# Kernel optimization log

Hardware: AMD Instinct MI355X
Metric: run time of the kernel (lower is better)

Reference implementation:

```python
import jax, jax.numpy as jnp
import numpy as np

FP8_MAX = 448.0  # max representable magnitude of float8_e4m3fn


def _quantize_tensorwise(x):
    """Tensor-wise fp8 quantization. Returns (fp8 tensor, inverse_scale) where
    dequant = fp8.astype(f32) * inverse_scale (matches Fp8Quantization.quantize_tensorwise)."""
    amax = jnp.max(jnp.abs(x))
    inv_scale = jnp.maximum(amax / FP8_MAX, jnp.float32(1e-12))
    q = (x / inv_scale).astype(jnp.float8_e4m3fn)
    return q, inv_scale


def _fp8_mm(qa, qb, sa, sb):
    # scaled fp8 GEMM: accumulate in f32, apply product of per-tensor inverse scales
    return (qa.astype(jnp.float32) @ qb.astype(jnp.float32)) * (sa * sb)


def setup_inputs() -> dict:
    key = jax.random.key(0)
    k1, k2, k3 = jax.random.split(key, 3)
    x = jax.random.normal(k1, (4, 2048, 2048), dtype=jnp.float32)
    weight = jax.random.normal(k2, (2048, 2048), dtype=jnp.float32) * 0.02
    bias = jax.random.normal(k3, (2048,), dtype=jnp.float32) * 0.01
    return {"x": x, "weight": weight, "bias": bias}


def reference(x, weight, bias):
    # flatten leading dims: inputmat = input.view(-1, K)
    K = x.shape[-1]
    xm = x.reshape(-1, K)                      # [T, K]
    qx, sx = _quantize_tensorwise(xm)          # fp8 input + inverse scale
    qwt, swt = _quantize_tensorwise(weight.T)  # fp8 weight^T [K, N] + inverse scale
    out = _fp8_mm(qx, qwt, sx, swt) + bias     # [T, N]
    return out.reshape(*x.shape[:-1], -1)
```

## Files before the change

kernel.cpp:

```cpp
#include <hip/hip_runtime.h>
#include <stdint.h>

typedef float f32x4 __attribute__((ext_vector_type(4)));
typedef int   i32x4 __attribute__((ext_vector_type(4)));
typedef int   i32x8 __attribute__((ext_vector_type(8)));

__global__ __launch_bounds__(256) void amax2_kernel(
    const float* __restrict__ x, int nx4,
    const float* __restrict__ w, int nw4,
    int xblocks, int* __restrict__ out) {
  const float4* src;
  int n4, j0, stride, slot;
  if ((int)blockIdx.x < xblocks) {
    src = (const float4*)x; n4 = nx4; slot = 0;
    j0 = blockIdx.x * blockDim.x + threadIdx.x;
    stride = xblocks * blockDim.x;
  } else {
    src = (const float4*)w; n4 = nw4; slot = 1;
    j0 = (blockIdx.x - xblocks) * blockDim.x + threadIdx.x;
    stride = (gridDim.x - xblocks) * blockDim.x;
  }
  float m = 0.f;
  for (int j = j0; j < n4; j += stride) {
    float4 v = src[j];
    m = fmaxf(m, fmaxf(fmaxf(fabsf(v.x), fabsf(v.y)),
                       fmaxf(fabsf(v.z), fabsf(v.w))));
  }
#pragma unroll
  for (int off = 32; off; off >>= 1)
    m = fmaxf(m, __shfl_down(m, off, 64));
  __shared__ float red[4];
  const int lane = threadIdx.x & 63;
  const int wv = threadIdx.x >> 6;
  if (lane == 0) red[wv] = m;
  __syncthreads();
  if (threadIdx.x == 0) {
    m = fmaxf(fmaxf(red[0], red[1]), fmaxf(red[2], red[3]));
    atomicMax(out + slot, (int)__float_as_uint(m));
  }
}

__global__ __launch_bounds__(256) void quant2_kernel(
    const float* __restrict__ x, unsigned char* __restrict__ qx, int nx4,
    const float* __restrict__ w, unsigned char* __restrict__ qw, int nw4,
    int xblocks, const unsigned* __restrict__ amax2) {
  const float4* src;
  unsigned* dst;
  int n4, j0, stride;
  float amax;
  if ((int)blockIdx.x < xblocks) {
    src = (const float4*)x; dst = (unsigned*)qx; n4 = nx4;
    amax = __uint_as_float(amax2[0]);
    j0 = blockIdx.x * blockDim.x + threadIdx.x;
    stride = xblocks * blockDim.x;
  } else {
    src = (const float4*)w; dst = (unsigned*)qw; n4 = nw4;
    amax = __uint_as_float(amax2[1]);
    j0 = (blockIdx.x - xblocks) * blockDim.x + threadIdx.x;
    stride = (gridDim.x - xblocks) * blockDim.x;
  }
  const float inv_scale = fmaxf(amax / 448.0f, 1e-12f);
  for (int j = j0; j < n4; j += stride) {
    float4 v = src[j];
    float a0 = v.x / inv_scale;
    float a1 = v.y / inv_scale;
    float a2 = v.z / inv_scale;
    float a3 = v.w / inv_scale;
    int p = 0;
    p = __builtin_amdgcn_cvt_pk_fp8_f32(a0, a1, p, false);
    p = __builtin_amdgcn_cvt_pk_fp8_f32(a2, a3, p, true);
    dst[j] = (unsigned)p;
  }
}

#define BM 128
#define BN 128
#define BK 128

__device__ __forceinline__ void load_lds16(const void* g, void* l) {
  __builtin_amdgcn_global_load_lds(
      (const __attribute__((address_space(1))) unsigned int*)g,
      (__attribute__((address_space(3))) unsigned int*)l, 16, 0, 0);
}

__global__ __launch_bounds__(256) void gemm_fp8_kernel(
    const unsigned char* __restrict__ Aq,
    const unsigned char* __restrict__ Bq,
    const float* __restrict__ bias,
    const unsigned* __restrict__ amax2,
    float* __restrict__ out,
    int T, int N, int K) {
  __shared__ __align__(16) unsigned char sA[BM * BK];
  __shared__ __align__(16) unsigned char sB[BN * BK];

  const int tid = threadIdx.x;
  const int lane = tid & 63;
  const int wave = tid >> 6;
  const int wm = (wave >> 1) * 64;
  const int wn = (wave & 1) * 64;
  const long m0 = (long)blockIdx.y * BM;
  const long n0 = (long)blockIdx.x * BN;

  f32x4 acc[4][4];
#pragma unroll
  for (int i = 0; i < 4; i++)
#pragma unroll
    for (int j = 0; j < 4; j++) acc[i][j] = (f32x4){0.f, 0.f, 0.f, 0.f};

  const int row_s = tid >> 3;
  const int c_s = tid & 7;
  const int scol = (c_s ^ (row_s & 7)) << 4;
  const int o = tid * 16;
  const unsigned char* aSrc[4];
  const unsigned char* bSrc[4];
#pragma unroll
  for (int r = 0; r < 4; r++) {
    aSrc[r] = Aq + (m0 + r * 32 + row_s) * (long)K + scol;
    bSrc[r] = Bq + (n0 + r * 32 + row_s) * (long)K + scol;
  }

  const int lm = lane & 15;
  const int q = lane >> 4;
  const int kc0 = q * 2;
  const int sxr = lm & 7;

  for (int k0 = 0; k0 < K; k0 += BK) {
#pragma unroll
    for (int r = 0; r < 4; r++) {
      load_lds16(aSrc[r] + k0, sA + r * 4096 + o);
      load_lds16(bSrc[r] + k0, sB + r * 4096 + o);
    }
    __syncthreads();

    i32x8 af[4], bf[4];
    const int c0 = (kc0 ^ sxr) << 4;
    const int c1 = ((kc0 + 1) ^ sxr) << 4;
#pragma unroll
    for (int mt = 0; mt < 4; mt++) {
      const unsigned char* p = sA + (wm + mt * 16 + lm) * BK;
      i32x4 lo = *(const i32x4*)(p + c0);
      i32x4 hi = *(const i32x4*)(p + c1);
      af[mt] = (i32x8){lo.x, lo.y, lo.z, lo.w, hi.x, hi.y, hi.z, hi.w};
    }
#pragma unroll
    for (int nt = 0; nt < 4; nt++) {
      const unsigned char* p = sB + (wn + nt * 16 + lm) * BK;
      i32x4 lo = *(const i32x4*)(p + c0);
      i32x4 hi = *(const i32x4*)(p + c1);
      bf[nt] = (i32x8){lo.x, lo.y, lo.z, lo.w, hi.x, hi.y, hi.z, hi.w};
    }
#pragma unroll
    for (int mt = 0; mt < 4; mt++)
#pragma unroll
      for (int nt = 0; nt < 4; nt++)
        acc[mt][nt] = __builtin_amdgcn_mfma_scale_f32_16x16x128_f8f6f4(
            af[mt], bf[nt], acc[mt][nt],
             0,  0,
             0, 0x7f7f7f7f,  0, 0x7f7f7f7f);
    __syncthreads();
  }

  const float sx = fmaxf(__uint_as_float(amax2[0]) / 448.0f, 1e-12f);
  const float sw = fmaxf(__uint_as_float(amax2[1]) / 448.0f, 1e-12f);
  const float scale = sx * sw;
  const int rbase = (lane >> 4) * 4;
#pragma unroll
  for (int mt = 0; mt < 4; mt++) {
#pragma unroll
    for (int r = 0; r < 4; r++) {
      const long row = m0 + wm + mt * 16 + rbase + r;
      float* orow = out + row * (long)N + n0 + wn;
#pragma unroll
      for (int nt = 0; nt < 4; nt++) {
        const int col = nt * 16 + lm;
        orow[col] = acc[mt][nt][r] * scale + bias[n0 + wn + col];
      }
    }
  }
}

extern "C" void kernel_launch(void* const* d_in, const int* in_sizes, int n_in,
                              void* d_out, int out_size, void* d_ws, size_t ws_size,
                              hipStream_t stream) {
  const float* x = (const float*)d_in[0];
  const float* w = (const float*)d_in[1];
  const float* bias = (const float*)d_in[2];
  float* out = (float*)d_out;

  const int N = in_sizes[2];
  const int K = in_sizes[1] / N;
  const int T = in_sizes[0] / K;

  unsigned* amax2 = (unsigned*)d_ws;
  unsigned char* qx = (unsigned char*)d_ws + 256;
  unsigned char* qw = qx + (size_t)T * K;

  const int XB = 1024;
  const int WB = 256;
  amax2_kernel<<<XB + WB, 256, 0, stream>>>(x, T * K / 4, w, N * K / 4, XB,
                                            (int*)amax2);
  quant2_kernel<<<XB + WB, 256, 0, stream>>>(x, qx, T * K / 4, w, qw, N * K / 4,
                                             XB, amax2);

  dim3 grid(N / BN, T / BM);
  gemm_fp8_kernel<<<grid, 256, 0, stream>>>(qx, qw, bias, amax2, out, T, N, K);
}
```

Before: 190.7 us.

## Rewrite fp8 GEMM as 256x256 tile with double-buffered LDS pipeline

```diff
diff --git a/kernel.cpp b/kernel.cpp
--- a/kernel.cpp
+++ b/kernel.cpp
@@ -73,9 +73,10 @@
   }
 }
 
-#define BM 128
-#define BN 128
+#define BM 256
+#define BN 256
 #define BK 128
+#define GEMM_LDS_BYTES (4 * 32768)
 
 __device__ __forceinline__ void load_lds16(const void* g, void* l) {
   __builtin_amdgcn_global_load_lds(
@@ -83,98 +84,158 @@
       (__attribute__((address_space(3))) unsigned int*)l, 16, 0, 0);
 }
 
-__global__ __launch_bounds__(256) void gemm_fp8_kernel(
+__global__ __launch_bounds__(512, 2) void gemm_fp8_kernel(
     const unsigned char* __restrict__ Aq,
     const unsigned char* __restrict__ Bq,
     const float* __restrict__ bias,
     const unsigned* __restrict__ amax2,
     float* __restrict__ out,
     int T, int N, int K) {
-  __shared__ __align__(16) unsigned char sA[BM * BK];
-  __shared__ __align__(16) unsigned char sB[BN * BK];
-
-  const int tid = threadIdx.x;
+  extern __shared__ unsigned char smem[];
+  unsigned char* sA = smem;
+  unsigned char* sB = smem + 65536;
+
+  const int tid  = threadIdx.x;
   const int lane = tid & 63;
   const int wave = tid >> 6;
-  const int wm = (wave >> 1) * 64;
-  const int wn = (wave & 1) * 64;
-  const long m0 = (long)blockIdx.y * BM;
-  const long n0 = (long)blockIdx.x * BN;
-
-  f32x4 acc[4][4];
-#pragma unroll
-  for (int i = 0; i < 4; i++)
-#pragma unroll
-    for (int j = 0; j < 4; j++) acc[i][j] = (f32x4){0.f, 0.f, 0.f, 0.f};
+  const int wm = (wave >> 2) * 128;
+  const int wn = (wave & 3) * 64;
+
+  int lin = (int)(blockIdx.y * gridDim.x + blockIdx.x);
+  const int nwg = (int)(gridDim.x * gridDim.y);
+  if ((nwg & 7) == 0) lin = (lin & 7) * (nwg >> 3) + (lin >> 3);
+  const long m0 = (long)(lin / (int)gridDim.x) * BM;
+  const long n0 = (long)(lin % (int)gridDim.x) * BN;
+
+  const long Kl = (long)K;
 
   const int row_s = tid >> 3;
-  const int c_s = tid & 7;
-  const int scol = (c_s ^ (row_s & 7)) << 4;
-  const int o = tid * 16;
-  const unsigned char* aSrc[4];
-  const unsigned char* bSrc[4];
-#pragma unroll
-  for (int r = 0; r < 4; r++) {
-    aSrc[r] = Aq + (m0 + r * 32 + row_s) * (long)K + scol;
-    bSrc[r] = Bq + (n0 + r * 32 + row_s) * (long)K + scol;
-  }
+  const int scol  = ((tid & 7) ^ (row_s & 7)) << 4;
+  const int t16   = tid << 4;
 
   const int lm = lane & 15;
-  const int q = lane >> 4;
-  const int kc0 = q * 2;
-  const int sxr = lm & 7;
-
-  for (int k0 = 0; k0 < K; k0 += BK) {
-#pragma unroll
-    for (int r = 0; r < 4; r++) {
-      load_lds16(aSrc[r] + k0, sA + r * 4096 + o);
-      load_lds16(bSrc[r] + k0, sB + r * 4096 + o);
-    }
-    __syncthreads();
-
-    i32x8 af[4], bf[4];
-    const int c0 = (kc0 ^ sxr) << 4;
-    const int c1 = ((kc0 + 1) ^ sxr) << 4;
-#pragma unroll
-    for (int mt = 0; mt < 4; mt++) {
-      const unsigned char* p = sA + (wm + mt * 16 + lm) * BK;
-      i32x4 lo = *(const i32x4*)(p + c0);
-      i32x4 hi = *(const i32x4*)(p + c1);
-      af[mt] = (i32x8){lo.x, lo.y, lo.z, lo.w, hi.x, hi.y, hi.z, hi.w};
-    }
-#pragma unroll
-    for (int nt = 0; nt < 4; nt++) {
-      const unsigned char* p = sB + (wn + nt * 16 + lm) * BK;
-      i32x4 lo = *(const i32x4*)(p + c0);
-      i32x4 hi = *(const i32x4*)(p + c1);
-      bf[nt] = (i32x8){lo.x, lo.y, lo.z, lo.w, hi.x, hi.y, hi.z, hi.w};
-    }
-#pragma unroll
-    for (int mt = 0; mt < 4; mt++)
-#pragma unroll
-      for (int nt = 0; nt < 4; nt++)
-        acc[mt][nt] = __builtin_amdgcn_mfma_scale_f32_16x16x128_f8f6f4(
-            af[mt], bf[nt], acc[mt][nt],
-             0,  0,
-             0, 0x7f7f7f7f,  0, 0x7f7f7f7f);
-    __syncthreads();
-  }
-
-  const float sx = fmaxf(__uint_as_float(amax2[0]) / 448.0f, 1e-12f);
-  const float sw = fmaxf(__uint_as_float(amax2[1]) / 448.0f, 1e-12f);
-  const float scale = sx * sw;
-  const int rbase = (lane >> 4) * 4;
-#pragma unroll
-  for (int mt = 0; mt < 4; mt++) {
-#pragma unroll
-    for (int r = 0; r < 4; r++) {
+  const int qh = lane >> 4;
+  const int c0 = ((qh * 2)     ^ (lm & 7)) << 4;
+  const int c1 = ((qh * 2 + 1) ^ (lm & 7)) << 4;
+
+  auto STAGE_A = [&](int Ts, int h) {
+    const unsigned char* g = Aq + (m0 + h * 128 + row_s) * Kl + (long)Ts * BK + scol;
+    unsigned char* l = sA + ((Ts & 1) << 15) + (h << 14) + t16;
+    load_lds16(g, l);
+    load_lds16(g + 64 * Kl, l + 8192);
+  };
+  auto STAGE_B = [&](int Ts, int h) {
+    const unsigned char* g = Bq + (n0 + h * 128 + row_s) * Kl + (long)Ts * BK + scol;
+    unsigned char* l = sB + ((Ts & 1) << 15) + (h << 14) + t16;
+    load_lds16(g, l);
+    load_lds16(g + 64 * Kl, l + 8192);
+  };
+  auto LDA = [&](const unsigned char* base, int mt) {
+    const unsigned char* p = base + (wm + mt * 16 + lm) * BK;
+    i32x4 lo = *(const i32x4*)(p + c0);
+    i32x4 hi = *(const i32x4*)(p + c1);
+    return (i32x8){lo.x, lo.y, lo.z, lo.w, hi.x, hi.y, hi.z, hi.w};
+  };
+  auto LDB = [&](const unsigned char* base, int nt) {
+    const unsigned char* p = base + (wn + nt * 16 + lm) * BK;
+    i32x4 lo = *(const i32x4*)(p + c0);
+    i32x4 hi = *(const i32x4*)(p + c1);
+    return (i32x8){lo.x, lo.y, lo.z, lo.w, hi.x, hi.y, hi.z, hi.w};
+  };
+
+  f32x4 acc[8][4];
+#pragma unroll
+  for (int i = 0; i < 8; ++i)
+#pragma unroll
+    for (int j = 0; j < 4; ++j) acc[i][j] = (f32x4){0.f, 0.f, 0.f, 0.f};
+
+  const int nt = K / BK;
+
+  STAGE_B(0, 0); STAGE_B(0, 1); STAGE_A(0, 0); STAGE_A(0, 1);
+  STAGE_B(1, 0); STAGE_B(1, 1);
+  asm volatile("s_waitcnt vmcnt(4)" ::: "memory");
+  __builtin_amdgcn_s_barrier();
+
+  i32x8 af[4], bf[4];
+  for (int t = 0; t < nt; ++t) {
+    const unsigned char* a = sA + ((t & 1) << 15);
+    const unsigned char* b = sB + ((t & 1) << 15);
+
+    af[0] = LDA(a, 0); af[1] = LDA(a, 1); af[2] = LDA(a, 2); af[3] = LDA(a, 3);
+    bf[0] = LDB(b, 0); bf[1] = LDB(b, 1);
+    if (t + 1 < nt) STAGE_A(t + 1, 0);
+    __builtin_amdgcn_s_barrier();
+    asm volatile("s_waitcnt lgkmcnt(0)");
+    __builtin_amdgcn_sched_barrier(0);
+    __builtin_amdgcn_s_setprio(1);
+#pragma unroll
+    for (int i = 0; i < 4; ++i)
+#pragma unroll
+      for (int j = 0; j < 2; ++j)
+        acc[i][j] = __builtin_amdgcn_mfma_scale_f32_16x16x128_f8f6f4(
+            af[i], bf[j], acc[i][j], 0, 0, 0, 0x7f7f7f7f, 0, 0x7f7f7f7f);
+    __builtin_amdgcn_s_setprio(0);
+    __builtin_amdgcn_s_barrier();
+
+    bf[2] = LDB(b, 2); bf[3] = LDB(b, 3);
+    if (t + 1 < nt) STAGE_A(t + 1, 1);
+    __builtin_amdgcn_s_barrier();
+    asm volatile("s_waitcnt lgkmcnt(0)");
+    __builtin_amdgcn_sched_barrier(0);
+    __builtin_amdgcn_s_setprio(1);
+#pragma unroll
+    for (int i = 0; i < 4; ++i)
+#pragma unroll
+      for (int j = 0; j < 2; ++j)
+        acc[i][2 + j] = __builtin_amdgcn_mfma_scale_f32_16x16x128_f8f6f4(
+            af[i], bf[2 + j], acc[i][2 + j], 0, 0, 0, 0x7f7f7f7f, 0, 0x7f7f7f7f);
+    __builtin_amdgcn_s_setprio(0);
+    __builtin_amdgcn_s_barrier();
+
+    af[0] = LDA(a, 4); af[1] = LDA(a, 5); af[2] = LDA(a, 6); af[3] = LDA(a, 7);
+    if (t + 2 < nt) STAGE_B(t + 2, 0);
+    __builtin_amdgcn_s_barrier();
+    asm volatile("s_waitcnt lgkmcnt(0)");
+    __builtin_amdgcn_sched_barrier(0);
+    __builtin_amdgcn_s_setprio(1);
+#pragma unroll
+    for (int i = 0; i < 4; ++i)
+#pragma unroll
+      for (int j = 0; j < 2; ++j)
+        acc[4 + i][j] = __builtin_amdgcn_mfma_scale_f32_16x16x128_f8f6f4(
+            af[i], bf[j], acc[4 + i][j], 0, 0, 0, 0x7f7f7f7f, 0, 0x7f7f7f7f);
+    __builtin_amdgcn_s_setprio(0);
+    __builtin_amdgcn_s_barrier();
+
+    if (t + 2 < nt) STAGE_B(t + 2, 1);
+    __builtin_amdgcn_s_setprio(1);
+#pragma unroll
+    for (int i = 0; i < 4; ++i)
+#pragma unroll
+      for (int j = 0; j < 2; ++j)
+        acc[4 + i][2 + j] = __builtin_amdgcn_mfma_scale_f32_16x16x128_f8f6f4(
+            af[i], bf[2 + j], acc[4 + i][2 + j], 0, 0, 0, 0x7f7f7f7f, 0, 0x7f7f7f7f);
+    __builtin_amdgcn_s_setprio(0);
+    asm volatile("s_waitcnt vmcnt(4)" ::: "memory");
+    __builtin_amdgcn_s_barrier();
+  }
+
+  const float fsx = fmaxf(__uint_as_float(amax2[0]) / 448.0f, 1e-12f);
+  const float fsw = fmaxf(__uint_as_float(amax2[1]) / 448.0f, 1e-12f);
+  const float scale = fsx * fsw;
+  const int rbase = qh * 4;
+  float bv[4];
+#pragma unroll
+  for (int j = 0; j < 4; ++j) bv[j] = bias[n0 + wn + j * 16 + lm];
+#pragma unroll
+  for (int mt = 0; mt < 8; ++mt) {
+#pragma unroll
+    for (int r = 0; r < 4; ++r) {
       const long row = m0 + wm + mt * 16 + rbase + r;
       float* orow = out + row * (long)N + n0 + wn;
 #pragma unroll
-      for (int nt = 0; nt < 4; nt++) {
-        const int col = nt * 16 + lm;
-        orow[col] = acc[mt][nt][r] * scale + bias[n0 + wn + col];
-      }
+      for (int j = 0; j < 4; ++j)
+        orow[j * 16 + lm] = acc[mt][j][r] * scale + bv[j];
     }
   }
 }
@@ -202,6 +263,14 @@
   quant2_kernel<<<XB + WB, 256, 0, stream>>>(x, qx, T * K / 4, w, qw, N * K / 4,
                                              XB, amax2);
 
+  static bool lds_attr_set = false;
+  if (!lds_attr_set) {
+    (void)hipFuncSetAttribute((const void*)gemm_fp8_kernel,
+                              hipFuncAttributeMaxDynamicSharedMemorySize,
+                              GEMM_LDS_BYTES);
+    lds_attr_set = true;
+  }
   dim3 grid(N / BN, T / BM);
-  gemm_fp8_kernel<<<grid, 256, 0, stream>>>(qx, qw, bias, amax2, out, T, N, K);
-}
+  gemm_fp8_kernel<<<grid, 512, GEMM_LDS_BYTES, stream>>>(qx, qw, bias, amax2,
+                                                         out, T, N, K);
+}
```

Measured after the change: 186.0 us. -2.5%, faster.
